# Performance work log

Measured on AMD Instinct MI355X. Metric: run time of the kernel, lower is better.

The kernel has to match this reference:

```python
import jax, jax.numpy as jnp
import numpy as np

NDIM = 3
IMG_SIZE = (192, 192, 192)
CPS = (5, 5, 5)
CP_GRID = (42, 42, 42)


def bspline_kernel_1d(stride):
    # cubic B-spline sampled at (i - radius)/stride, length 4*stride-1
    n = 4 * stride - 1
    t = np.abs((np.arange(n) - n // 2) / float(stride))
    vals = np.where(t < 1.0, 2.0 / 3.0 + (0.5 * t - 1.0) * t ** 2,
                    np.where(t < 2.0, -((t - 2.0) ** 3) / 6.0, 0.0))
    return jnp.asarray(vals, dtype=jnp.float32)


def conv_transpose1d_lastaxis(x, kernel, stride, padding):
    # depthwise transposed conv along last axis; same kernel for every channel,
    # so fold all leading dims into the batch and use a single-channel conv
    # with lhs_dilation (equivalent to conv_transpose; kernel is symmetric).
    shp = x.shape
    K = kernel.shape[0]
    x2 = x.reshape(-1, 1, shp[-1])  # [N, C=1, L]
    w = kernel.reshape(1, 1, K)     # [O, I, W]
    pad = K - 1 - padding
    y = jax.lax.conv_general_dilated(
        x2, w, window_strides=(1,), padding=[(pad, pad)],
        lhs_dilation=(stride,), dimension_numbers=("NCW", "OIW", "NCW"))
    return y.reshape(shp[:-1] + (y.shape[-1],))


def setup_inputs() -> dict:
    key = jax.random.key(0)
    v = jax.random.normal(key, (4, NDIM) + CP_GRID, dtype=jnp.float32)
    return {"v": v}


def reference(v) -> jnp.ndarray:
    kernels = [bspline_kernel_1d(s) for s in CPS]
    for i in range(NDIM):
        k = kernels[i]
        s = CPS[i]
        p = (k.shape[0] - 1) // 2
        x = jnp.moveaxis(v, i + 2, -1)
        x = conv_transpose1d_lastaxis(x, k, s, p)
        v = jnp.moveaxis(x, -1, i + 2)
    # crop: slice(s, s + img_size) per spatial dim
    slicer = (slice(None), slice(None)) + tuple(
        slice(CPS[i], CPS[i] + IMG_SIZE[i]) for i in range(NDIM))
    return v[slicer]
```

## Files before the change

### kernel.cpp

```cpp
#include <hip/hip_runtime.h>


#define CPN 42
#define IMG 192
#define NTHREADS 256
#define SLICE (CPN * CPN * CPN)
#define PLANE (CPN * CPN)
#define NBLK (12 * IMG)

typedef float v4f __attribute__((ext_vector_type(4)));

__device__ __forceinline__ float bsp_w_rt(int r, int d) {
  double f = (double)r / 5.0;
  double g = (double)(5 - r) / 5.0;
  double w;
  if (d == 0)      { w = g * g * g / 6.0; }
  else if (d == 1) { w = 2.0 / 3.0 + (0.5 * f - 1.0) * f * f; }
  else if (d == 2) { w = 2.0 / 3.0 + (0.5 * g - 1.0) * g * g; }
  else             { w = f * f * f / 6.0; }
  return (float)w;
}

__global__ void __launch_bounds__(NTHREADS) ffd_kernel(
    const float* __restrict__ v, float* __restrict__ out) {
  const int tid = threadIdx.x;
  const int bid = blockIdx.x;
  const int n  = (bid & 7) * (NBLK / 8) + (bid >> 3);
  const int sl = n / IMG;
  const int x  = n - sl * IMG;
  const int ax = x / 5;
  const int rx = x - 5 * ax;

  __shared__ v4f  wq[5];
  __shared__ float t1[PLANE];
  __shared__ float t2[IMG * CPN];

  if (tid < 5) {
    v4f qv;
    qv.x = bsp_w_rt(tid, 0); qv.y = bsp_w_rt(tid, 1);
    qv.z = bsp_w_rt(tid, 2); qv.w = bsp_w_rt(tid, 3);
    wq[tid] = qv;
  }

  const int w    = tid >> 6;
  const int lane = tid & 63;
  const int q    = lane < 48 ? lane : 47;
  const int c0   = (4 * q) / 5;
  float wz[4][5];
#pragma unroll
  for (int k = 0; k < 4; ++k) {
    int z = 4 * q + k;
    int c = z / 5;
    int r = z - 5 * c;
    int off = c - c0;
#pragma unroll
    for (int t = 0; t < 5; ++t) {
      int d = t - off;
      wz[k][t] = (d >= 0 && d < 4) ? bsp_w_rt(r, d) : 0.0f;
    }
  }
  __syncthreads();

  const float* vp0 = v + (size_t)sl * SLICE + (size_t)ax * PLANE;
  const v4f wx = wq[rx];
  for (int l = tid; l < PLANE; l += NTHREADS) {
    float a = wx.x * vp0[l];
    a = fmaf(wx.y, vp0[l + PLANE], a);
    a = fmaf(wx.z, vp0[l + 2 * PLANE], a);
    a = fmaf(wx.w, vp0[l + 3 * PLANE], a);
    t1[l] = a;
  }
  __syncthreads();

  for (int l = tid; l < IMG * CPN; l += NTHREADS) {
    int y  = l / CPN;
    int cz = l - y * CPN;
    int ay = y / 5;
    int ry = y - 5 * ay;
    v4f wy = wq[ry];
    const float* tp = &t1[ay * CPN + cz];
    float a = wy.x * tp[0];
    a = fmaf(wy.y, tp[CPN], a);
    a = fmaf(wy.z, tp[2 * CPN], a);
    a = fmaf(wy.w, tp[3 * CPN], a);
    t2[l] = a;
  }
  __syncthreads();

  float* ob = out + (size_t)n * (IMG * IMG);
  for (int i = 0; i < 48; ++i) {
    int y = w + 4 * i;
    const float* tp = &t2[y * CPN + c0];
    float s0 = tp[0], s1 = tp[1], s2 = tp[2], s3 = tp[3], s4 = tp[4];
    v4f res;
#pragma unroll
    for (int k = 0; k < 4; ++k) {
      float a = wz[k][0] * s0;
      a = fmaf(wz[k][1], s1, a);
      a = fmaf(wz[k][2], s2, a);
      a = fmaf(wz[k][3], s3, a);
      a = fmaf(wz[k][4], s4, a);
      res[k] = a;
    }
    if (lane < 48)
      *reinterpret_cast<v4f*>(ob + y * IMG + 4 * q) = res;
  }
}

extern "C" void kernel_launch(void* const* d_in, const int* in_sizes, int n_in,
                              void* d_out, int out_size, void* d_ws, size_t ws_size,
                              hipStream_t stream) {
  (void)in_sizes; (void)n_in; (void)d_ws; (void)ws_size; (void)out_size;
  const float* v = (const float*)d_in[0];
  float* out = (float*)d_out;
  ffd_kernel<<<dim3(NBLK), NTHREADS, 0, stream>>>(v, out);
}
```

Measured before the change: 349.8 us.

## Double-buffer y-pass output in row chunks to shrink LDS and overlap stages

Replaces the full 192x42 shared y-pass buffer with two 24-row chunk buffers. The y-pass for the next chunk is computed while the z-pass of the current chunk is writing output, with one barrier per chunk. This cuts LDS use per block, which may allow more resident blocks, and interleaves LDS compute with global stores. The cost is more barriers (8 instead of 1).

```diff
diff --git a/kernel.cpp b/kernel.cpp
--- a/kernel.cpp
+++ b/kernel.cpp
@@ -7,6 +7,8 @@
 #define SLICE (CPN * CPN * CPN)
 #define PLANE (CPN * CPN)
 #define NBLK (12 * IMG)
+#define CHY 24
+#define NCH (IMG / CHY)
 
 typedef float v4f __attribute__((ext_vector_type(4)));
 
@@ -33,7 +35,7 @@
 
   __shared__ v4f  wq[5];
   __shared__ float t1[PLANE];
-  __shared__ float t2[IMG * CPN];
+  __shared__ float t2c[2][CHY * CPN];
 
   if (tid < 5) {
     v4f qv;
@@ -72,9 +74,10 @@
   }
   __syncthreads();
 
-  for (int l = tid; l < IMG * CPN; l += NTHREADS) {
-    int y  = l / CPN;
-    int cz = l - y * CPN;
+  for (int l = tid; l < CHY * CPN; l += NTHREADS) {
+    int yy = l / CPN;
+    int cz = l - yy * CPN;
+    int y  = yy;
     int ay = y / 5;
     int ry = y - 5 * ay;
     v4f wy = wq[ry];
@@ -83,27 +86,50 @@
     a = fmaf(wy.y, tp[CPN], a);
     a = fmaf(wy.z, tp[2 * CPN], a);
     a = fmaf(wy.w, tp[3 * CPN], a);
-    t2[l] = a;
+    t2c[0][l] = a;
   }
   __syncthreads();
 
   float* ob = out + (size_t)n * (IMG * IMG);
-  for (int i = 0; i < 48; ++i) {
-    int y = w + 4 * i;
-    const float* tp = &t2[y * CPN + c0];
-    float s0 = tp[0], s1 = tp[1], s2 = tp[2], s3 = tp[3], s4 = tp[4];
-    v4f res;
+  for (int j = 0; j < NCH; ++j) {
+    const float* buf = t2c[j & 1];
 #pragma unroll
-    for (int k = 0; k < 4; ++k) {
-      float a = wz[k][0] * s0;
-      a = fmaf(wz[k][1], s1, a);
-      a = fmaf(wz[k][2], s2, a);
-      a = fmaf(wz[k][3], s3, a);
-      a = fmaf(wz[k][4], s4, a);
-      res[k] = a;
+    for (int i = 0; i < CHY / 4; ++i) {
+      int yy = w + 4 * i;
+      int y  = j * CHY + yy;
+      const float* tp = &buf[yy * CPN + c0];
+      float s0 = tp[0], s1 = tp[1], s2 = tp[2], s3 = tp[3], s4 = tp[4];
+      v4f res;
+#pragma unroll
+      for (int k = 0; k < 4; ++k) {
+        float a = wz[k][0] * s0;
+        a = fmaf(wz[k][1], s1, a);
+        a = fmaf(wz[k][2], s2, a);
+        a = fmaf(wz[k][3], s3, a);
+        a = fmaf(wz[k][4], s4, a);
+        res[k] = a;
+      }
+      if (lane < 48)
+        *reinterpret_cast<v4f*>(ob + y * IMG + 4 * q) = res;
     }
-    if (lane < 48)
-      *reinterpret_cast<v4f*>(ob + y * IMG + 4 * q) = res;
+    if (j + 1 < NCH) {
+      float* nbuf = t2c[(j + 1) & 1];
+      for (int l = tid; l < CHY * CPN; l += NTHREADS) {
+        int yy = l / CPN;
+        int cz = l - yy * CPN;
+        int y  = (j + 1) * CHY + yy;
+        int ay = y / 5;
+        int ry = y - 5 * ay;
+        v4f wy = wq[ry];
+        const float* tp = &t1[ay * CPN + cz];
+        float a = wy.x * tp[0];
+        a = fmaf(wy.y, tp[CPN], a);
+        a = fmaf(wy.z, tp[2 * CPN], a);
+        a = fmaf(wy.w, tp[3 * CPN], a);
+        nbuf[l] = a;
+      }
+    }
+    __syncthreads();
   }
 }
 
```

After: 347.1 us. No clear change (-0.8%).
